# Kernel optimization log

Hardware: AMD Instinct MI355X
Metric: run time of the kernel (lower is better)

Reference implementation:

```python
import jax, jax.numpy as jnp
import numpy as np

B, H, S, D = 2, 16, 2048, 64

def setup_inputs() -> dict:
    key = jax.random.key(0)
    kq, kk, kv = jax.random.split(key, 3)
    query = jax.random.normal(kq, (B, H, S, D), dtype=jnp.float32)
    k = jax.random.normal(kk, (B, H, S, D), dtype=jnp.float32)
    value = jax.random.normal(kv, (B, H, S, D), dtype=jnp.float32)
    return {"query": query, "key": k, "value": value}

def reference(query, key, value):
    d_k = query.shape[-1]
    scale = 1.0 / jnp.sqrt(jnp.asarray(d_k, dtype=jnp.float32))
    # scores: [B, H, S, S]
    scores = jnp.einsum('bhqd,bhkd->bhqk', query, key) * scale
    attn = jax.nn.softmax(scores, axis=-1)
    # output: [B, H, S, D]
    return jnp.einsum('bhqk,bhkd->bhqd', attn, value)
```

## Files before the change

### kernel.cpp

```cpp
#include <hip/hip_runtime.h>
#include <hip/hip_bf16.h>

#define S_LEN 2048
#define HD    64
#define BH    32
#define KVB   64
#define NIT   (S_LEN / KVB)
#define ELEMS_PER_ARR (BH * S_LEN * HD)

typedef __attribute__((ext_vector_type(8)))  short bf16x8;
typedef __attribute__((ext_vector_type(4)))  float f32x4;
typedef __attribute__((ext_vector_type(16))) float f32x16;

union FragU { unsigned u[4]; bf16x8 v; };

__device__ __forceinline__ unsigned cvtpk(float lo, float hi) {
  unsigned r;
  asm("v_cvt_pk_bf16_f32 %0, %1, %2" : "=v"(r) : "v"(lo), "v"(hi));
  return r;
}

__device__ __forceinline__ f32x4 mfma16(bf16x8 a, bf16x8 b, f32x4 c) {
  return __builtin_amdgcn_mfma_f32_16x16x32_bf16(a, b, c, 0, 0, 0);
}
__device__ __forceinline__ f32x16 mfma32(bf16x8 a, bf16x8 b, f32x16 c) {
  return __builtin_amdgcn_mfma_f32_32x32x16_bf16(a, b, c, 0, 0, 0);
}

template <int B>
__device__ __forceinline__ void pack_chunk(const f32x16& s, FragU& p) {
  unsigned wA = cvtpk(s[B + 0], s[B + 1]);
  unsigned wB = cvtpk(s[B + 2], s[B + 3]);
  unsigned wC = cvtpk(s[B + 4], s[B + 5]);
  unsigned wD = cvtpk(s[B + 6], s[B + 7]);
  asm("v_permlane32_swap_b32 %0, %1" : "+v"(wA), "+v"(wC));
  asm("v_permlane32_swap_b32 %0, %1" : "+v"(wB), "+v"(wD));
  p.u[0] = wA; p.u[1] = wB; p.u[2] = wC; p.u[3] = wD;
}

__global__ __launch_bounds__(256) void cvt_k(
    const float* __restrict__ K, unsigned short* __restrict__ Kb) {
  const size_t i = ((size_t)blockIdx.x * 256 + threadIdx.x) * 8;
  float4 a = *(const float4*)(K + i);
  float4 b = *(const float4*)(K + i + 4);
  uint4 w;
  w.x = cvtpk(a.x, a.y); w.y = cvtpk(a.z, a.w);
  w.z = cvtpk(b.x, b.y); w.w = cvtpk(b.z, b.w);
  *(uint4*)(Kb + i) = w;
}

__global__ __launch_bounds__(256) void transpose_v(
    const float* __restrict__ V, unsigned short* __restrict__ Vt) {
  __shared__ float T[64 * 68];
  const int tid = threadIdx.x;
  const int bh = blockIdx.x >> 5;
  const int s0 = (blockIdx.x & 31) * 64;
  const float* vb = V + ((size_t)bh * S_LEN + s0) * HD;
  {
    const int r = tid >> 4, c4 = (tid & 15) * 4;
#pragma unroll
    for (int i = 0; i < 4; ++i) {
      float4 x = *(const float4*)(vb + (size_t)(r + 16 * i) * HD + c4);
      *(float4*)&T[(r + 16 * i) * 68 + c4] = x;
    }
  }
  __syncthreads();
  const int d = tid >> 2, sc = (tid & 3) * 16;
  unsigned short* out = Vt + (size_t)bh * HD * S_LEN + (size_t)d * S_LEN + s0 + sc;
  uint4 w0, w1;
  w0.x = cvtpk(T[(sc + 0) * 68 + d], T[(sc + 1) * 68 + d]);
  w0.y = cvtpk(T[(sc + 2) * 68 + d], T[(sc + 3) * 68 + d]);
  w0.z = cvtpk(T[(sc + 4) * 68 + d], T[(sc + 5) * 68 + d]);
  w0.w = cvtpk(T[(sc + 6) * 68 + d], T[(sc + 7) * 68 + d]);
  w1.x = cvtpk(T[(sc + 8) * 68 + d], T[(sc + 9) * 68 + d]);
  w1.y = cvtpk(T[(sc + 10) * 68 + d], T[(sc + 11) * 68 + d]);
  w1.z = cvtpk(T[(sc + 12) * 68 + d], T[(sc + 13) * 68 + d]);
  w1.w = cvtpk(T[(sc + 14) * 68 + d], T[(sc + 15) * 68 + d]);
  *(uint4*)out = w0;
  *(uint4*)(out + 8) = w1;
}

__global__ __launch_bounds__(256, 2) void sdpa_main32(
    const float* __restrict__ Q, const unsigned short* __restrict__ Kb,
    const unsigned short* __restrict__ Vt, float* __restrict__ O) {
  __shared__ __align__(16) unsigned short Klds[2][KVB * 64];
  __shared__ __align__(16) unsigned short Vlds[2][HD * KVB];

  const int tid  = threadIdx.x;
  const int lane = tid & 63;
  const int wv   = tid >> 6;
  const int q31  = lane & 31;
  const int hi   = lane >> 5;
  const int r7   = q31 & 7;

  const int bid  = blockIdx.x;
  const int obid = (bid & 7) * 64 + (bid >> 3);
  const int bh   = obid >> 4;
  const int qblk = obid & 15;
  const int q0   = qblk * 128 + wv * 32;

  const float* Qp = Q + (size_t)bh * S_LEN * HD;
  const unsigned short* Kp = Kb + (size_t)bh * S_LEN * HD;
  const unsigned short* Vp = Vt + (size_t)bh * HD * S_LEN;
  float* Op = O + (size_t)bh * S_LEN * HD;

  const float qs = 0.125f * 1.44269504088896340736f;
  FragU qb[4];
  {
    const float* qrow = Qp + (size_t)(q0 + q31) * HD + 8 * hi;
#pragma unroll
    for (int dc = 0; dc < 4; ++dc) {
      float4 a = *(const float4*)(qrow + dc * 16);
      float4 b = *(const float4*)(qrow + dc * 16 + 4);
      qb[dc].u[0] = cvtpk(a.x * qs, a.y * qs);
      qb[dc].u[1] = cvtpk(a.z * qs, a.w * qs);
      qb[dc].u[2] = cvtpk(b.x * qs, b.y * qs);
      qb[dc].u[3] = cvtpk(b.z * qs, b.w * qs);
    }
  }

  const int rk  = tid >> 2;
  const int qq  = (tid & 3) * 16;
  const int rr7 = rk & 7;
  const int wb0 = rk * 64 + (((qq >> 3)) ^ rr7) * 8;
  const int wb1 = rk * 64 + (((qq >> 3) | 1) ^ rr7) * 8;

  bf16x8 sK0 = *(const bf16x8*)(Kp + (size_t)rk * HD + qq);
  bf16x8 sK1 = *(const bf16x8*)(Kp + (size_t)rk * HD + qq + 8);
  bf16x8 sV0 = *(const bf16x8*)(Vp + (size_t)rk * S_LEN + qq);
  bf16x8 sV1 = *(const bf16x8*)(Vp + (size_t)rk * S_LEN + qq + 8);
  *(bf16x8*)&Klds[0][wb0] = sK0;
  *(bf16x8*)&Klds[0][wb1] = sK1;
  *(bf16x8*)&Vlds[0][wb0] = sV0;
  *(bf16x8*)&Vlds[0][wb1] = sV1;
  __syncthreads();

  const f32x16 z16 = {0,0,0,0, 0,0,0,0, 0,0,0,0, 0,0,0,0};
  f32x16 acc0 = z16, acc1 = z16;
  float m = -__builtin_inff();
  float l = 0.f;
  int cur = 0;

  for (int it = 0; it < NIT; ++it) {
    const bool more = (it + 1) < NIT;
    const int ktn = (it + 1) * KVB;
    if (more) {
      sK0 = *(const bf16x8*)(Kp + (size_t)(ktn + rk) * HD + qq);
      sK1 = *(const bf16x8*)(Kp + (size_t)(ktn + rk) * HD + qq + 8);
      sV0 = *(const bf16x8*)(Vp + (size_t)rk * S_LEN + ktn + qq);
      sV1 = *(const bf16x8*)(Vp + (size_t)rk * S_LEN + ktn + qq + 8);
    }
    const bf16x8* K8 = (const bf16x8*)&Klds[cur][0];
    const bf16x8* V8 = (const bf16x8*)&Vlds[cur][0];

    f32x16 st0 = z16, st1 = z16;
    __builtin_amdgcn_s_setprio(1);
#pragma unroll
    for (int dc = 0; dc < 4; ++dc) {
      const int slot = (2 * dc + hi) ^ r7;
      bf16x8 ka0 = K8[q31 * 8 + slot];
      bf16x8 ka1 = K8[(32 + q31) * 8 + slot];
      st0 = mfma32(ka0, qb[dc].v, st0);
      st1 = mfma32(ka1, qb[dc].v, st1);
    }
    __builtin_amdgcn_s_setprio(0);

    float tm = fmaxf(
        fmaxf(fmaxf(fmaxf(st0[0], st0[1]), fmaxf(st0[2], st0[3])),
              fmaxf(fmaxf(st0[4], st0[5]), fmaxf(st0[6], st0[7]))),
        fmaxf(fmaxf(fmaxf(st0[8], st0[9]), fmaxf(st0[10], st0[11])),
              fmaxf(fmaxf(st0[12], st0[13]), fmaxf(st0[14], st0[15]))));
    tm = fmaxf(tm, fmaxf(
        fmaxf(fmaxf(fmaxf(st1[0], st1[1]), fmaxf(st1[2], st1[3])),
              fmaxf(fmaxf(st1[4], st1[5]), fmaxf(st1[6], st1[7]))),
        fmaxf(fmaxf(fmaxf(st1[8], st1[9]), fmaxf(st1[10], st1[11])),
              fmaxf(fmaxf(st1[12], st1[13]), fmaxf(st1[14], st1[15])))));
    tm = fmaxf(tm, __shfl_xor(tm, 32));

    if (__any(tm > m + 8.0f)) {
      const float mn = fmaxf(m, tm);
      const float alpha = __builtin_amdgcn_exp2f(m - mn);
      m = mn;
      l *= alpha;
      acc0 *= alpha;
      acc1 *= alpha;
    }

    float rs = 0.f;
#pragma unroll
    for (int j = 0; j < 16; ++j) {
      st0[j] = __builtin_amdgcn_exp2f(st0[j] - m);
      rs += st0[j];
    }
#pragma unroll
    for (int j = 0; j < 16; ++j) {
      st1[j] = __builtin_amdgcn_exp2f(st1[j] - m);
      rs += st1[j];
    }
    rs += __shfl_xor(rs, 32);
    l += rs;

    FragU pb[4];
    pack_chunk<0>(st0, pb[0]);
    pack_chunk<8>(st0, pb[1]);
    pack_chunk<0>(st1, pb[2]);
    pack_chunk<8>(st1, pb[3]);

    __builtin_amdgcn_s_setprio(1);
#pragma unroll
    for (int c = 0; c < 4; ++c) {
      const int slot = (2 * c + hi) ^ r7;
      bf16x8 va0 = V8[q31 * 8 + slot];
      bf16x8 va1 = V8[(32 + q31) * 8 + slot];
      acc0 = mfma32(va0, pb[c].v, acc0);
      acc1 = mfma32(va1, pb[c].v, acc1);
    }
    __builtin_amdgcn_s_setprio(0);

    if (more) {
      *(bf16x8*)&Klds[cur ^ 1][wb0] = sK0;
      *(bf16x8*)&Klds[cur ^ 1][wb1] = sK1;
      *(bf16x8*)&Vlds[cur ^ 1][wb0] = sV0;
      *(bf16x8*)&Vlds[cur ^ 1][wb1] = sV1;
    }
    __syncthreads();
    cur ^= 1;
  }

  const float inv = 1.0f / l;
  float* orow = Op + (size_t)(q0 + q31) * HD + 4 * hi;
#pragma unroll
  for (int u = 0; u < 4; ++u) {
    float4 o;
    o.x = acc0[4 * u + 0] * inv; o.y = acc0[4 * u + 1] * inv;
    o.z = acc0[4 * u + 2] * inv; o.w = acc0[4 * u + 3] * inv;
    *(float4*)(orow + 8 * u) = o;
  }
#pragma unroll
  for (int u = 0; u < 4; ++u) {
    float4 o;
    o.x = acc1[4 * u + 0] * inv; o.y = acc1[4 * u + 1] * inv;
    o.z = acc1[4 * u + 2] * inv; o.w = acc1[4 * u + 3] * inv;
    *(float4*)(orow + 32 + 8 * u) = o;
  }
}

#define KROW 72
#define VROW 40
__device__ __forceinline__ void redist(const f32x4& pa, const f32x4& pc,
                                       int srcA, unsigned sel, FragU& pb) {
  unsigned pk0 = cvtpk(pa[0], pc[0]);
  unsigned pk1 = cvtpk(pa[1], pc[1]);
  unsigned pk2 = cvtpk(pa[2], pc[2]);
  unsigned pk3 = cvtpk(pa[3], pc[3]);
  unsigned w0 = (unsigned)__shfl((int)pk0, srcA);
  unsigned w1 = (unsigned)__shfl((int)pk1, srcA);
  unsigned w2 = (unsigned)__shfl((int)pk2, srcA);
  unsigned w3 = (unsigned)__shfl((int)pk3, srcA);
  unsigned w4 = (unsigned)__shfl((int)pk0, srcA + 16);
  unsigned w5 = (unsigned)__shfl((int)pk1, srcA + 16);
  unsigned w6 = (unsigned)__shfl((int)pk2, srcA + 16);
  unsigned w7 = (unsigned)__shfl((int)pk3, srcA + 16);
  pb.u[0] = __builtin_amdgcn_perm(w1, w0, sel);
  pb.u[1] = __builtin_amdgcn_perm(w3, w2, sel);
  pb.u[2] = __builtin_amdgcn_perm(w5, w4, sel);
  pb.u[3] = __builtin_amdgcn_perm(w7, w6, sel);
}

__global__ __launch_bounds__(256) void sdpa_fallback(
    const float* __restrict__ Q, const float* __restrict__ K,
    const float* __restrict__ V, float* __restrict__ O) {
  __shared__ __align__(16) unsigned short Klds[32 * KROW];
  __shared__ __align__(16) unsigned short Vlds[HD * VROW];
  const int tid = threadIdx.x;
  const int lane = tid & 63;
  const int wv = tid >> 6;
  const int g = lane >> 4;
  const int q15 = lane & 15;
  const int bh = blockIdx.x >> 5;
  const int qblk = blockIdx.x & 31;
  const int qt = qblk * 64 + wv * 16;
  const size_t base = (size_t)bh * S_LEN * HD;
  const float* Qp = Q + base;
  const float* Kp = K + base;
  const float* Vp = V + base;
  float* Op = O + base;
  const float qs = 0.125f * 1.44269504088896340736f;
  FragU qf0, qf1;
  {
    const float* qrow = Qp + (size_t)(qt + q15) * HD + 8 * g;
    float4 a = *(const float4*)(qrow);
    float4 b = *(const float4*)(qrow + 4);
    qf0.u[0] = cvtpk(a.x * qs, a.y * qs); qf0.u[1] = cvtpk(a.z * qs, a.w * qs);
    qf0.u[2] = cvtpk(b.x * qs, b.y * qs); qf0.u[3] = cvtpk(b.z * qs, b.w * qs);
    a = *(const float4*)(qrow + 32);
    b = *(const float4*)(qrow + 36);
    qf1.u[0] = cvtpk(a.x * qs, a.y * qs); qf1.u[1] = cvtpk(a.z * qs, a.w * qs);
    qf1.u[2] = cvtpk(b.x * qs, b.y * qs); qf1.u[3] = cvtpk(b.z * qs, b.w * qs);
  }
  f32x4 acc0 = {0.f,0.f,0.f,0.f};
  f32x4 acc1 = acc0, acc2 = acc0, acc3 = acc0;
  float m = -__builtin_inff();
  float l = 0.f;
  const int srcA = 32 * (g & 1) + q15;
  const unsigned sel = (g >= 2) ? 0x07060302u : 0x05040100u;
  const int sk = tid >> 3;
  const int sd = (tid & 7) * 8;
  const bf16x8* Kv = (const bf16x8*)Klds;
  const bf16x8* Vv = (const bf16x8*)Vlds;
  for (int kt = 0; kt < S_LEN; kt += 32) {
    __syncthreads();
    {
      const float* p = Kp + (size_t)(kt + sk) * HD + sd;
      float4 a = *(const float4*)p;
      float4 b = *(const float4*)(p + 4);
      uint4 w;
      w.x = cvtpk(a.x, a.y); w.y = cvtpk(a.z, a.w);
      w.z = cvtpk(b.x, b.y); w.w = cvtpk(b.z, b.w);
      *(uint4*)&Klds[sk * KROW + sd] = w;
    }
    {
      const float* p = Vp + (size_t)(kt + sk) * HD + sd;
      float4 a = *(const float4*)p;
      float4 b = *(const float4*)(p + 4);
      unsigned u0 = cvtpk(a.x, a.y), u1 = cvtpk(a.z, a.w);
      unsigned u2 = cvtpk(b.x, b.y), u3 = cvtpk(b.z, b.w);
      Vlds[(sd + 0) * VROW + sk] = (unsigned short)(u0 & 0xffffu);
      Vlds[(sd + 1) * VROW + sk] = (unsigned short)(u0 >> 16);
      Vlds[(sd + 2) * VROW + sk] = (unsigned short)(u1 & 0xffffu);
      Vlds[(sd + 3) * VROW + sk] = (unsigned short)(u1 >> 16);
      Vlds[(sd + 4) * VROW + sk] = (unsigned short)(u2 & 0xffffu);
      Vlds[(sd + 5) * VROW + sk] = (unsigned short)(u2 >> 16);
      Vlds[(sd + 6) * VROW + sk] = (unsigned short)(u3 & 0xffffu);
      Vlds[(sd + 7) * VROW + sk] = (unsigned short)(u3 >> 16);
    }
    __syncthreads();
    f32x4 st0 = {0.f,0.f,0.f,0.f}, st1 = st0;
    {
      bf16x8 kfa = Kv[q15 * 9 + g];
      bf16x8 kfb = Kv[q15 * 9 + 4 + g];
      st0 = mfma16(kfa, qf0.v, st0);
      st0 = mfma16(kfb, qf1.v, st0);
      bf16x8 kfc = Kv[(16 + q15) * 9 + g];
      bf16x8 kfd = Kv[(16 + q15) * 9 + 4 + g];
      st1 = mfma16(kfc, qf0.v, st1);
      st1 = mfma16(kfd, qf1.v, st1);
    }
    float tm = fmaxf(fmaxf(fmaxf(st0[0], st0[1]), fmaxf(st0[2], st0[3])),
                     fmaxf(fmaxf(st1[0], st1[1]), fmaxf(st1[2], st1[3])));
    tm = fmaxf(tm, __shfl_xor(tm, 16));
    tm = fmaxf(tm, __shfl_xor(tm, 32));
    const float mn = fmaxf(m, tm);
    const float alpha = __builtin_amdgcn_exp2f(m - mn);
    m = mn;
    float rs = 0.f;
#pragma unroll
    for (int r = 0; r < 4; ++r) {
      st0[r] = __builtin_amdgcn_exp2f(st0[r] - mn);
      st1[r] = __builtin_amdgcn_exp2f(st1[r] - mn);
      rs += st0[r] + st1[r];
    }
    rs += __shfl_xor(rs, 16);
    rs += __shfl_xor(rs, 32);
    l = l * alpha + rs;
    acc0 *= alpha; acc1 *= alpha; acc2 *= alpha; acc3 *= alpha;
    FragU pb;
    redist(st0, st1, srcA, sel, pb);
    {
      bf16x8 vf0 = Vv[q15 * 5 + g];
      bf16x8 vf1 = Vv[(16 + q15) * 5 + g];
      bf16x8 vf2 = Vv[(32 + q15) * 5 + g];
      bf16x8 vf3 = Vv[(48 + q15) * 5 + g];
      acc0 = mfma16(vf0, pb.v, acc0);
      acc1 = mfma16(vf1, pb.v, acc1);
      acc2 = mfma16(vf2, pb.v, acc2);
      acc3 = mfma16(vf3, pb.v, acc3);
    }
  }
  const float inv = 1.0f / l;
  float* orow = Op + (size_t)(qt + q15) * HD + 4 * g;
  float4 o;
  o.x = acc0[0]*inv; o.y = acc0[1]*inv; o.z = acc0[2]*inv; o.w = acc0[3]*inv;
  *(float4*)(orow +  0) = o;
  o.x = acc1[0]*inv; o.y = acc1[1]*inv; o.z = acc1[2]*inv; o.w = acc1[3]*inv;
  *(float4*)(orow + 16) = o;
  o.x = acc2[0]*inv; o.y = acc2[1]*inv; o.z = acc2[2]*inv; o.w = acc2[3]*inv;
  *(float4*)(orow + 32) = o;
  o.x = acc3[0]*inv; o.y = acc3[1]*inv; o.z = acc3[2]*inv; o.w = acc3[3]*inv;
  *(float4*)(orow + 48) = o;
}

extern "C" void kernel_launch(void* const* d_in, const int* in_sizes, int n_in,
                              void* d_out, int out_size, void* d_ws, size_t ws_size,
                              hipStream_t stream) {
  const float* Q = (const float*)d_in[0];
  const float* K = (const float*)d_in[1];
  const float* V = (const float*)d_in[2];
  float* O = (float*)d_out;
  const size_t need = (size_t)2 * ELEMS_PER_ARR * 2;
  if (ws_size >= need) {
    unsigned short* Kb = (unsigned short*)d_ws;
    unsigned short* Vt = Kb + ELEMS_PER_ARR;
    cvt_k<<<2048, 256, 0, stream>>>(K, Kb);
    transpose_v<<<1024, 256, 0, stream>>>(V, Vt);
    sdpa_main32<<<512, 256, 0, stream>>>(Q, Kb, Vt, O);
  } else {
    sdpa_fallback<<<1024, 256, 0, stream>>>(Q, K, V, O);
  }
}
```

Before: 142.5 us.

## Split KV sequence across two wave groups per block and merge partial softmax

```diff
diff --git a/kernel.cpp b/kernel.cpp
--- a/kernel.cpp
+++ b/kernel.cpp
@@ -5,7 +5,7 @@
 #define HD    64
 #define BH    32
 #define KVB   64
-#define NIT   (S_LEN / KVB)
+#define NIT_H (1024 / KVB)
 #define ELEMS_PER_ARR (BH * S_LEN * HD)
 
 typedef __attribute__((ext_vector_type(8)))  short bf16x8;
@@ -80,15 +80,16 @@
   *(uint4*)(out + 8) = w1;
 }
 
-__global__ __launch_bounds__(256, 2) void sdpa_main32(
+__global__ __launch_bounds__(512, 4) void sdpa_main32s(
     const float* __restrict__ Q, const unsigned short* __restrict__ Kb,
     const unsigned short* __restrict__ Vt, float* __restrict__ O) {
-  __shared__ __align__(16) unsigned short Klds[2][KVB * 64];
-  __shared__ __align__(16) unsigned short Vlds[2][HD * KVB];
+  __shared__ __align__(16) unsigned short SMEM[32768];
 
   const int tid  = threadIdx.x;
   const int lane = tid & 63;
   const int wv   = tid >> 6;
+  const int half = wv >> 2;
+  const int wq   = wv & 3;
   const int q31  = lane & 31;
   const int hi   = lane >> 5;
   const int r7   = q31 & 7;
@@ -97,7 +98,7 @@
   const int obid = (bid & 7) * 64 + (bid >> 3);
   const int bh   = obid >> 4;
   const int qblk = obid & 15;
-  const int q0   = qblk * 128 + wv * 32;
+  const int q0   = qblk * 128 + wq * 32;
 
   const float* Qp = Q + (size_t)bh * S_LEN * HD;
   const unsigned short* Kp = Kb + (size_t)bh * S_LEN * HD;
@@ -119,20 +120,26 @@
     }
   }
 
-  const int rk  = tid >> 2;
-  const int qq  = (tid & 3) * 16;
-  const int rr7 = rk & 7;
-  const int wb0 = rk * 64 + (((qq >> 3)) ^ rr7) * 8;
-  const int wb1 = rk * 64 + (((qq >> 3) | 1) ^ rr7) * 8;
-
-  bf16x8 sK0 = *(const bf16x8*)(Kp + (size_t)rk * HD + qq);
-  bf16x8 sK1 = *(const bf16x8*)(Kp + (size_t)rk * HD + qq + 8);
-  bf16x8 sV0 = *(const bf16x8*)(Vp + (size_t)rk * S_LEN + qq);
-  bf16x8 sV1 = *(const bf16x8*)(Vp + (size_t)rk * S_LEN + qq + 8);
-  *(bf16x8*)&Klds[0][wb0] = sK0;
-  *(bf16x8*)&Klds[0][wb1] = sK1;
-  *(bf16x8*)&Vlds[0][wb0] = sV0;
-  *(bf16x8*)&Vlds[0][wb1] = sV1;
+  const int sh    = tid >> 8;
+  const int tid2  = tid & 255;
+  const int rk    = tid2 >> 2;
+  const int qq    = (tid2 & 3) * 16;
+  const int rr7   = rk & 7;
+  const int wb0   = rk * 64 + (((qq >> 3)) ^ rr7) * 8;
+  const int wb1   = rk * 64 + (((qq >> 3) | 1) ^ rr7) * 8;
+  const int skv   = sh * 1024;
+
+  bf16x8 sK0 = *(const bf16x8*)(Kp + (size_t)(skv + rk) * HD + qq);
+  bf16x8 sK1 = *(const bf16x8*)(Kp + (size_t)(skv + rk) * HD + qq + 8);
+  bf16x8 sV0 = *(const bf16x8*)(Vp + (size_t)rk * S_LEN + skv + qq);
+  bf16x8 sV1 = *(const bf16x8*)(Vp + (size_t)rk * S_LEN + skv + qq + 8);
+  {
+    unsigned short* reg0 = SMEM + (sh * 2 + 0) * 8192;
+    *(bf16x8*)&reg0[wb0]        = sK0;
+    *(bf16x8*)&reg0[wb1]        = sK1;
+    *(bf16x8*)&reg0[4096 + wb0] = sV0;
+    *(bf16x8*)&reg0[4096 + wb1] = sV1;
+  }
   __syncthreads();
 
   const f32x16 z16 = {0,0,0,0, 0,0,0,0, 0,0,0,0, 0,0,0,0};
@@ -141,17 +148,17 @@
   float l = 0.f;
   int cur = 0;
 
-  for (int it = 0; it < NIT; ++it) {
-    const bool more = (it + 1) < NIT;
-    const int ktn = (it + 1) * KVB;
+  for (int it = 0; it < NIT_H; ++it) {
+    const bool more = (it + 1) < NIT_H;
+    const int ktn = skv + (it + 1) * KVB;
     if (more) {
       sK0 = *(const bf16x8*)(Kp + (size_t)(ktn + rk) * HD + qq);
       sK1 = *(const bf16x8*)(Kp + (size_t)(ktn + rk) * HD + qq + 8);
       sV0 = *(const bf16x8*)(Vp + (size_t)rk * S_LEN + ktn + qq);
       sV1 = *(const bf16x8*)(Vp + (size_t)rk * S_LEN + ktn + qq + 8);
     }
-    const bf16x8* K8 = (const bf16x8*)&Klds[cur][0];
-    const bf16x8* V8 = (const bf16x8*)&Vlds[cur][0];
+    const bf16x8* K8 = (const bf16x8*)(SMEM + (half * 2 + cur) * 8192);
+    const bf16x8* V8 = (const bf16x8*)(SMEM + (half * 2 + cur) * 8192 + 4096);
 
     f32x16 st0 = z16, st1 = z16;
     __builtin_amdgcn_s_setprio(1);
@@ -197,7 +204,6 @@
       st1[j] = __builtin_amdgcn_exp2f(st1[j] - m);
       rs += st1[j];
     }
-    rs += __shfl_xor(rs, 32);
     l += rs;
 
     FragU pb[4];
@@ -218,30 +224,57 @@
     __builtin_amdgcn_s_setprio(0);
 
     if (more) {
-      *(bf16x8*)&Klds[cur ^ 1][wb0] = sK0;
-      *(bf16x8*)&Klds[cur ^ 1][wb1] = sK1;
-      *(bf16x8*)&Vlds[cur ^ 1][wb0] = sV0;
-      *(bf16x8*)&Vlds[cur ^ 1][wb1] = sV1;
+      unsigned short* regn = SMEM + (sh * 2 + (cur ^ 1)) * 8192;
+      *(bf16x8*)&regn[wb0]        = sK0;
+      *(bf16x8*)&regn[wb1]        = sK1;
+      *(bf16x8*)&regn[4096 + wb0] = sV0;
+      *(bf16x8*)&regn[4096 + wb1] = sV1;
     }
     __syncthreads();
     cur ^= 1;
   }
 
-  const float inv = 1.0f / l;
-  float* orow = Op + (size_t)(q0 + q31) * HD + 4 * hi;
-#pragma unroll
-  for (int u = 0; u < 4; ++u) {
-    float4 o;
-    o.x = acc0[4 * u + 0] * inv; o.y = acc0[4 * u + 1] * inv;
-    o.z = acc0[4 * u + 2] * inv; o.w = acc0[4 * u + 3] * inv;
-    *(float4*)(orow + 8 * u) = o;
-  }
-#pragma unroll
-  for (int u = 0; u < 4; ++u) {
-    float4 o;
-    o.x = acc1[4 * u + 0] * inv; o.y = acc1[4 * u + 1] * inv;
-    o.z = acc1[4 * u + 2] * inv; o.w = acc1[4 * u + 3] * inv;
-    *(float4*)(orow + 32 + 8 * u) = o;
+  l += __shfl_xor(l, 32);
+
+  __syncthreads();
+  float* A = (float*)SMEM;
+  if (half == 1) {
+    float* dst = A + (size_t)(wq * 64 + lane) * 34;
+#pragma unroll
+    for (int j = 0; j < 16; ++j) dst[j] = acc0[j];
+#pragma unroll
+    for (int j = 0; j < 16; ++j) dst[16 + j] = acc1[j];
+    dst[32] = m;
+    dst[33] = l;
+  }
+  __syncthreads();
+  if (half == 0) {
+    const float* src = A + (size_t)(wq * 64 + lane) * 34;
+    const float mP = src[32], lP = src[33];
+    const float ms = fmaxf(m, mP);
+    const float a0 = __builtin_amdgcn_exp2f(m - ms);
+    const float a1 = __builtin_amdgcn_exp2f(mP - ms);
+    const float lc = l * a0 + lP * a1;
+    const float inv = 1.0f / lc;
+    float* orow = Op + (size_t)(q0 + q31) * HD + 4 * hi;
+#pragma unroll
+    for (int u = 0; u < 4; ++u) {
+      float4 o;
+      o.x = (acc0[4 * u + 0] * a0 + src[4 * u + 0] * a1) * inv;
+      o.y = (acc0[4 * u + 1] * a0 + src[4 * u + 1] * a1) * inv;
+      o.z = (acc0[4 * u + 2] * a0 + src[4 * u + 2] * a1) * inv;
+      o.w = (acc0[4 * u + 3] * a0 + src[4 * u + 3] * a1) * inv;
+      *(float4*)(orow + 8 * u) = o;
+    }
+#pragma unroll
+    for (int u = 0; u < 4; ++u) {
+      float4 o;
+      o.x = (acc1[4 * u + 0] * a0 + src[16 + 4 * u + 0] * a1) * inv;
+      o.y = (acc1[4 * u + 1] * a0 + src[16 + 4 * u + 1] * a1) * inv;
+      o.z = (acc1[4 * u + 2] * a0 + src[16 + 4 * u + 2] * a1) * inv;
+      o.w = (acc1[4 * u + 3] * a0 + src[16 + 4 * u + 3] * a1) * inv;
+      *(float4*)(orow + 32 + 8 * u) = o;
+    }
   }
 }
 
@@ -403,7 +436,7 @@
     unsigned short* Vt = Kb + ELEMS_PER_ARR;
     cvt_k<<<2048, 256, 0, stream>>>(K, Kb);
     transpose_v<<<1024, 256, 0, stream>>>(V, Vt);
-    sdpa_main32<<<512, 256, 0, stream>>>(Q, Kb, Vt, O);
+    sdpa_main32s<<<512, 512, 0, stream>>>(Q, Kb, Vt, O);
   } else {
     sdpa_fallback<<<1024, 256, 0, stream>>>(Q, K, V, O);
   }
```

Result: no change. 142.2 us (-0.2%).
